# Kernel tuning notes

Measured on AMD Instinct MI355X. Metric: run time of the kernel, lower is better.

## Reference

```python
import jax, jax.numpy as jnp
import numpy as np

N_NODES = 50000
N_EDGES = 800000
IN_DIM = 256
HIDDEN = 32
HEADS = 4
OUT_DIM = 64


def setup_inputs() -> dict:
    key = jax.random.key(0)
    k1, k2, k3, k4, k5, k6, k7 = jax.random.split(key, 7)
    h = jax.random.normal(k1, (N_NODES, IN_DIM), dtype=jnp.float32)
    src = jax.random.randint(k2, (N_EDGES,), 0, N_NODES, dtype=jnp.int32)
    dst = jax.random.randint(k3, (N_EDGES,), 0, N_NODES, dtype=jnp.int32)
    # xavier_normal with relu gain, per-head weights
    gain = float(np.sqrt(2.0))
    W1 = gain * jnp.sqrt(2.0 / (IN_DIM + HIDDEN)) * jax.random.normal(k4, (HEADS, IN_DIM, HIDDEN), dtype=jnp.float32)
    a1 = gain * jnp.sqrt(2.0 / (2 * HIDDEN + 1)) * jax.random.normal(k5, (HEADS, 2 * HIDDEN), dtype=jnp.float32)
    W2 = gain * jnp.sqrt(2.0 / (HIDDEN * HEADS + OUT_DIM)) * jax.random.normal(k6, (1, HIDDEN * HEADS, OUT_DIM), dtype=jnp.float32)
    a2 = gain * jnp.sqrt(2.0 / (2 * OUT_DIM + 1)) * jax.random.normal(k7, (1, 2 * OUT_DIM), dtype=jnp.float32)
    return {"h": h, "src": src, "dst": dst, "W1": W1, "a1": a1, "W2": W2, "a2": a2}


def _gat_layer(x, src, dst, W, a):
    # x: [N, in], W: [H, in, d], a: [H, 2d]
    N = x.shape[0]
    d = W.shape[-1]
    z = jnp.einsum('ni,hio->nho', x, W)                    # [N, H, d]
    a_s, a_d = a[:, :d], a[:, d:]
    es = jnp.einsum('nho,ho->nh', z, a_s)                  # per-node src score
    ed = jnp.einsum('nho,ho->nh', z, a_d)                  # per-node dst score
    e = jax.nn.leaky_relu(es[src] + ed[dst])               # [E, H]
    # segment (per-destination) softmax over incoming edges
    emax = jax.ops.segment_max(e, dst, num_segments=N)     # [N, H]
    ex = jnp.exp(e - emax[dst])
    denom = jax.ops.segment_sum(ex, dst, num_segments=N)   # [N, H]
    alpha = ex / denom[dst]                                # [E, H]
    # scatter weighted sum of source feats back to destinations
    out = jax.ops.segment_sum(alpha[:, :, None] * z[src], dst, num_segments=N)  # [N, H, d]
    return out.reshape(N, -1)


def reference(h, src, dst, W1, a1, W2, a2):
    h1 = jax.nn.elu(_gat_layer(h, src, dst, W1, a1))       # [N, HEADS*HIDDEN]
    return _gat_layer(h1, src, dst, W2, a2)                # [N, OUT_DIM]
```

## Files before the change

kernel.cpp:

```cpp
#include <hip/hip_runtime.h>
#include <hip/hip_bf16.h>
#include <math.h>

#define N_NODES 50000
#define N_EDGES 800000
#define IN_DIM 256
#define HID 32
#define HEADS 4
#define OUT_DIM 64

#define SCAN_CHUNK 1024
#define SCAN_BLOCKS ((N_NODES + SCAN_CHUNK - 1) / SCAN_CHUNK)

typedef __attribute__((ext_vector_type(8))) short bf16x8;
typedef __attribute__((ext_vector_type(4))) float f32x4;

__device__ __forceinline__ float lrelu(float e) { return e > 0.f ? e : 0.01f * e; }
__device__ __forceinline__ float bflo(unsigned u) { return __uint_as_float(u << 16); }
__device__ __forceinline__ float bfhi(unsigned u) { return __uint_as_float(u & 0xffff0000u); }

__device__ __forceinline__ unsigned short rne_bf16(float x) {
    unsigned u = __float_as_uint(x);
    unsigned r = u + 0x7fffu + ((u >> 16) & 1u);
    return (unsigned short)(r >> 16);
}

__device__ __forceinline__ void splitf(float x, short& hi, short& lo) {
    unsigned u = __float_as_uint(x);
    unsigned short h = (unsigned short)(u >> 16);
    float hf = __uint_as_float(((unsigned)h) << 16);
    float l = x - hf;
    unsigned short lb = (unsigned short)(__float_as_uint(l) >> 16);
    hi = (short)h;
    lo = (short)lb;
}


__global__ void __launch_bounds__(256) prep_kernel(
        const float* __restrict__ W1, const float* __restrict__ a1,
        const float* __restrict__ W2, const float* __restrict__ a2,
        unsigned short* __restrict__ B1h, unsigned short* __restrict__ B1l,
        unsigned short* __restrict__ B2h, unsigned short* __restrict__ B2l,
        int* __restrict__ count) {
    int gid = blockIdx.x * 256 + threadIdx.x;
    if (gid < N_NODES) count[gid] = 0;

    int k = blockIdx.x;
    int c = threadIdx.x;
    if (c < 144) {
        float val = 0.f;
        if (c < 128) {
            val = W1[(size_t)(c >> 5) * IN_DIM * HID + (size_t)k * HID + (c & 31)];
        } else if (c < 136) {
            int j = c - 128;
            int hd = (j < 4) ? j : (j - 4);
            int off = (j < 4) ? 0 : HID;
            const float* Wp = W1 + (size_t)hd * IN_DIM * HID + (size_t)k * HID;
            const float* ap = a1 + hd * 2 * HID + off;
            float s = 0.f;
            for (int o = 0; o < HID; o++) s += Wp[o] * ap[o];
            val = s;
        }
        unsigned short hi = rne_bf16(val);
        float hf = __uint_as_float(((unsigned)hi) << 16);
        unsigned short lo = rne_bf16(val - hf);
        int s_ = k >> 5, q = (k >> 3) & 3, j8 = k & 7;
        int nt = c >> 4, L = q * 16 + (c & 15);
        size_t idx = (((size_t)s_ * 9 + nt) * 64 + L) * 8 + j8;
        B1h[idx] = hi;
        B1l[idx] = lo;
    } else if (c >= 160 && c < 240 && k < 128) {
        int c2 = c - 160;
        float val = 0.f;
        if (c2 < 64) {
            val = W2[(size_t)k * OUT_DIM + c2];
        } else if (c2 < 66) {
            const float* ap = a2 + (c2 - 64) * OUT_DIM;
            const float* Wp = W2 + (size_t)k * OUT_DIM;
            float s = 0.f;
            for (int o = 0; o < OUT_DIM; o++) s += Wp[o] * ap[o];
            val = s;
        }
        unsigned short hi = rne_bf16(val);
        float hf = __uint_as_float(((unsigned)hi) << 16);
        unsigned short lo = rne_bf16(val - hf);
        int s_ = k >> 5, q = (k >> 3) & 3, j8 = k & 7;
        int nt = c2 >> 4, L = q * 16 + (c2 & 15);
        size_t idx = (((size_t)s_ * 5 + nt) * 64 + L) * 8 + j8;
        B2h[idx] = hi;
        B2l[idx] = lo;
    }
}


__global__ void hist_kernel(const int* __restrict__ dst, int* __restrict__ count,
                            int* __restrict__ rank) {
    int i = blockIdx.x * blockDim.x + threadIdx.x;
    if (i < N_EDGES) rank[i] = atomicAdd(&count[dst[i]], 1);
}

__global__ void scan1_kernel(const int* __restrict__ count, int* __restrict__ row_start,
                             int* __restrict__ blocksum) {
    __shared__ int sdata[256];
    int t = threadIdx.x;
    int base = blockIdx.x * SCAN_CHUNK + t * 4;
    int v[4];
    int s = 0;
#pragma unroll
    for (int j = 0; j < 4; j++) {
        int idx = base + j;
        int x = (idx < N_NODES) ? count[idx] : 0;
        v[j] = x;
        s += x;
    }
    sdata[t] = s;
    __syncthreads();
    for (int off = 1; off < 256; off <<= 1) {
        int u = (t >= off) ? sdata[t - off] : 0;
        __syncthreads();
        sdata[t] += u;
        __syncthreads();
    }
    int excl = sdata[t] - s;
#pragma unroll
    for (int j = 0; j < 4; j++) {
        int idx = base + j;
        if (idx < N_NODES) row_start[idx] = excl;
        excl += v[j];
    }
    if (t == 255) blocksum[blockIdx.x] = sdata[255];
}

__global__ void scan23_kernel(int* __restrict__ row_start, const int* __restrict__ blocksum) {
    __shared__ int pre;
    int t = threadIdx.x;
    if (t < 64) {
        int v = (t < SCAN_BLOCKS) ? blocksum[t] : 0;
#pragma unroll
        for (int off = 1; off < 64; off <<= 1) {
            int u = __shfl_up(v, off);
            if (t >= off) v += u;
        }
        if (t == blockIdx.x) pre = v - blocksum[t];
    }
    __syncthreads();
    int add = pre;
    int base = blockIdx.x * SCAN_CHUNK + t * 4;
#pragma unroll
    for (int j = 0; j < 4; j++) {
        int idx = base + j;
        if (idx < N_NODES) row_start[idx] += add;
    }
}

__global__ void scatter_kernel(const int* __restrict__ src, const int* __restrict__ dst,
                               const int* __restrict__ rank, const int* __restrict__ row_start,
                               int* __restrict__ esrc) {
    int i = blockIdx.x * blockDim.x + threadIdx.x;
    if (i < N_EDGES) esrc[row_start[dst[i]] + rank[i]] = src[i];
}


__global__ void __launch_bounds__(256) proj1_mfma(
        const float* __restrict__ h, const unsigned short* __restrict__ Bh,
        const unsigned short* __restrict__ Bl, __hip_bfloat16* __restrict__ z1b,
        float* __restrict__ es1, float* __restrict__ ed1) {
    int tid = threadIdx.x;
    int wave = tid >> 6;
    int L = tid & 63;
    int q = L >> 4, L15 = L & 15;
    int n0 = blockIdx.x * 64 + wave * 16;

    int rowA = n0 + L15;
    int rrA = rowA < N_NODES ? rowA : N_NODES - 1;
    const float* hrow = h + (size_t)rrA * IN_DIM + q * 8;

    f32x4 acc[9];
#pragma unroll
    for (int nt = 0; nt < 9; nt++) acc[nt] = (f32x4)(0.f);

    float4 x0 = *(const float4*)(hrow);
    float4 x1 = *(const float4*)(hrow + 4);

#pragma unroll
    for (int s = 0; s < 8; s++) {
        int sn = (s < 7) ? s + 1 : 7;
        float4 p0 = *(const float4*)(hrow + sn * 32);
        float4 p1 = *(const float4*)(hrow + sn * 32 + 4);

        float xs[8] = {x0.x, x0.y, x0.z, x0.w, x1.x, x1.y, x1.z, x1.w};
        bf16x8 ah, al;
#pragma unroll
        for (int j = 0; j < 8; j++) {
            short hi, lo;
            splitf(xs[j], hi, lo);
            ah[j] = hi;
            al[j] = lo;
        }

        const bf16x8* bhp = (const bf16x8*)(Bh + ((size_t)s * 9 * 64) * 8 + (size_t)L * 8);
        const bf16x8* blp = (const bf16x8*)(Bl + ((size_t)s * 9 * 64) * 8 + (size_t)L * 8);
#pragma unroll
        for (int nt = 0; nt < 9; nt++) {
            bf16x8 bh = bhp[nt * 64];
            acc[nt] = __builtin_amdgcn_mfma_f32_16x16x32_bf16(ah, bh, acc[nt], 0, 0, 0);
            acc[nt] = __builtin_amdgcn_mfma_f32_16x16x32_bf16(al, bh, acc[nt], 0, 0, 0);
        }
        {
            bf16x8 bl8 = blp[8 * 64];
            acc[8] = __builtin_amdgcn_mfma_f32_16x16x32_bf16(ah, bl8, acc[8], 0, 0, 0);
        }
        x0 = p0;
        x1 = p1;
    }

#pragma unroll
    for (int r = 0; r < 4; r++) {
        int rowc = n0 + q * 4 + r;
        if (rowc < N_NODES) {
#pragma unroll
            for (int nt = 0; nt < 8; nt++)
                z1b[(size_t)rowc * 128 + nt * 16 + L15] = __float2bfloat16(acc[nt][r]);
            if (L15 < 4) es1[rowc * HEADS + L15] = acc[8][r];
            else if (L15 < 8) ed1[rowc * HEADS + (L15 - 4)] = acc[8][r];
        }
    }
}


__global__ void __launch_bounds__(256) agg1_kernel(
        const __hip_bfloat16* __restrict__ z1b, const float* __restrict__ es1,
        const float* __restrict__ ed1, const int* __restrict__ row_start,
        const int* __restrict__ count, const int* __restrict__ esrc,
        __hip_bfloat16* __restrict__ h1b) {
    int v = blockIdx.x * 4 + (threadIdx.x >> 6);
    int L = threadIdx.x & 63;
    int sub = L >> 4;
    int c16 = L & 15;
    int hd = c16 >> 2;
    int beg = row_start[v], deg = count[v];
    float edv = ed1[v * HEADS + hd];
    const int* ep = esrc + beg;
    float lacc = 0.f;
    float acc[8];
#pragma unroll
    for (int i = 0; i < 8; i++) acc[i] = 0.f;
    const uint4* zq = (const uint4*)z1b;

    for (int j0 = 0; j0 < deg; j0 += 32) {
        int se[8];
        uint4 u[8];
        float ev[8];
#pragma unroll
        for (int g = 0; g < 8; g++) {
            if (j0 + g * 4 < deg) {
                int e = j0 + g * 4 + sub;
                se[g] = ep[(e < deg) ? e : 0];
            }
        }
#pragma unroll
        for (int g = 0; g < 8; g++) {
            if (j0 + g * 4 < deg) {
                u[g] = zq[(size_t)se[g] * 16 + c16];
                ev[g] = es1[se[g] * HEADS + hd];
            }
        }
#pragma unroll
        for (int g = 0; g < 8; g++) {
            if (j0 + g * 4 < deg) {
                bool val = (j0 + g * 4 + sub) < deg;
                float q = val ? __expf(lrelu(ev[g] + edv)) : 0.f;
                lacc += q;
                acc[0] = fmaf(q, bflo(u[g].x), acc[0]);
                acc[1] = fmaf(q, bfhi(u[g].x), acc[1]);
                acc[2] = fmaf(q, bflo(u[g].y), acc[2]);
                acc[3] = fmaf(q, bfhi(u[g].y), acc[3]);
                acc[4] = fmaf(q, bflo(u[g].z), acc[4]);
                acc[5] = fmaf(q, bfhi(u[g].z), acc[5]);
                acc[6] = fmaf(q, bflo(u[g].w), acc[6]);
                acc[7] = fmaf(q, bfhi(u[g].w), acc[7]);
            }
        }
    }
    lacc += __shfl_xor(lacc, 1);
    lacc += __shfl_xor(lacc, 2);
    lacc += __shfl_xor(lacc, 16);
    lacc += __shfl_xor(lacc, 32);
    lacc *= 0.25f;
#pragma unroll
    for (int i = 0; i < 8; i++) {
        acc[i] += __shfl_xor(acc[i], 16);
        acc[i] += __shfl_xor(acc[i], 32);
    }
    if (L < 16) {
        float inv = (deg > 0) ? 1.f / lacc : 0.f;
        unsigned w[4];
#pragma unroll
        for (int i = 0; i < 4; i++) {
            float r0 = acc[2 * i] * inv;
            float r1 = acc[2 * i + 1] * inv;
            r0 = r0 > 0.f ? r0 : __expf(r0) - 1.f;
            r1 = r1 > 0.f ? r1 : __expf(r1) - 1.f;
            w[i] = (unsigned)rne_bf16(r0) | ((unsigned)rne_bf16(r1) << 16);
        }
        uint4* dst = (uint4*)(h1b + (size_t)v * 128 + c16 * 8);
        *dst = make_uint4(w[0], w[1], w[2], w[3]);
    }
}


__global__ void __launch_bounds__(256) proj2_mfma(
        const __hip_bfloat16* __restrict__ h1b, const unsigned short* __restrict__ Bh,
        const unsigned short* __restrict__ Bl, __hip_bfloat16* __restrict__ z2b,
        float* __restrict__ es2, float* __restrict__ ed2) {
    int tid = threadIdx.x;
    int wave = tid >> 6;
    int L = tid & 63;
    int q = L >> 4, L15 = L & 15;
    int n0 = blockIdx.x * 64 + wave * 16;

    int rowA = n0 + L15;
    int rrA = rowA < N_NODES ? rowA : N_NODES - 1;
    const bf16x8* hq = (const bf16x8*)(h1b + (size_t)rrA * 128);

    f32x4 acc[5];
#pragma unroll
    for (int nt = 0; nt < 5; nt++) acc[nt] = (f32x4)(0.f);

#pragma unroll
    for (int s = 0; s < 4; s++) {
        bf16x8 a = hq[s * 4 + q];
        const bf16x8* bhp = (const bf16x8*)(Bh + ((size_t)s * 5 * 64) * 8 + (size_t)L * 8);
        const bf16x8* blp = (const bf16x8*)(Bl + ((size_t)s * 5 * 64) * 8 + (size_t)L * 8);
#pragma unroll
        for (int nt = 0; nt < 5; nt++)
            acc[nt] = __builtin_amdgcn_mfma_f32_16x16x32_bf16(a, bhp[nt * 64], acc[nt], 0, 0, 0);
        acc[4] = __builtin_amdgcn_mfma_f32_16x16x32_bf16(a, blp[4 * 64], acc[4], 0, 0, 0);
    }

#pragma unroll
    for (int r = 0; r < 4; r++) {
        int rowc = n0 + q * 4 + r;
        if (rowc < N_NODES) {
#pragma unroll
            for (int nt = 0; nt < 4; nt++)
                z2b[(size_t)rowc * OUT_DIM + nt * 16 + L15] = __float2bfloat16(acc[nt][r]);
            if (L15 == 0) es2[rowc] = acc[4][r];
            else if (L15 == 1) ed2[rowc] = acc[4][r];
        }
    }
}


__global__ void __launch_bounds__(256) agg2_kernel(
        const __hip_bfloat16* __restrict__ z2b, const float* __restrict__ es2,
        const float* __restrict__ ed2, const int* __restrict__ row_start,
        const int* __restrict__ count, const int* __restrict__ esrc,
        float* __restrict__ out) {
    int v = blockIdx.x * 4 + (threadIdx.x >> 6);
    int L = threadIdx.x & 63;
    int sub = L >> 3;
    int c8 = L & 7;
    int beg = row_start[v], deg = count[v];
    float edv = ed2[v];
    const int* ep = esrc + beg;
    float lacc = 0.f;
    float acc[8];
#pragma unroll
    for (int i = 0; i < 8; i++) acc[i] = 0.f;
    const uint4* zq = (const uint4*)z2b;

    for (int j0 = 0; j0 < deg; j0 += 32) {
        int se[4];
        uint4 u[4];
        float ev[4];
#pragma unroll
        for (int g = 0; g < 4; g++) {
            if (j0 + g * 8 < deg) {
                int e = j0 + g * 8 + sub;
                se[g] = ep[(e < deg) ? e : 0];
            }
        }
#pragma unroll
        for (int g = 0; g < 4; g++) {
            if (j0 + g * 8 < deg) {
                u[g] = zq[(size_t)se[g] * 8 + c8];
                ev[g] = es2[se[g]];
            }
        }
#pragma unroll
        for (int g = 0; g < 4; g++) {
            if (j0 + g * 8 < deg) {
                bool val = (j0 + g * 8 + sub) < deg;
                float q = val ? __expf(lrelu(ev[g] + edv)) : 0.f;
                lacc += q;
                acc[0] = fmaf(q, bflo(u[g].x), acc[0]);
                acc[1] = fmaf(q, bfhi(u[g].x), acc[1]);
                acc[2] = fmaf(q, bflo(u[g].y), acc[2]);
                acc[3] = fmaf(q, bfhi(u[g].y), acc[3]);
                acc[4] = fmaf(q, bflo(u[g].z), acc[4]);
                acc[5] = fmaf(q, bfhi(u[g].z), acc[5]);
                acc[6] = fmaf(q, bflo(u[g].w), acc[6]);
                acc[7] = fmaf(q, bfhi(u[g].w), acc[7]);
            }
        }
    }
    lacc += __shfl_xor(lacc, 8);
    lacc += __shfl_xor(lacc, 16);
    lacc += __shfl_xor(lacc, 32);
#pragma unroll
    for (int i = 0; i < 8; i++) {
        acc[i] += __shfl_xor(acc[i], 8);
        acc[i] += __shfl_xor(acc[i], 16);
        acc[i] += __shfl_xor(acc[i], 32);
    }
    if (L < 8) {
        float inv = (deg > 0) ? 1.f / lacc : 0.f;
        float4 r0, r1;
#pragma unroll
        for (int i = 0; i < 8; i++) {
            float r = acc[i] * inv;
            if (i < 4) (&r0.x)[i] = r;
            else (&r1.x)[i - 4] = r;
        }
        float* dst = out + (size_t)v * OUT_DIM + c8 * 8;
        *(float4*)dst = r0;
        *(float4*)(dst + 4) = r1;
    }
}


extern "C" void kernel_launch(void* const* d_in, const int* in_sizes, int n_in,
                              void* d_out, int out_size, void* d_ws, size_t ws_size,
                              hipStream_t stream) {
    const float* h  = (const float*)d_in[0];
    const int* src  = (const int*)d_in[1];
    const int* dst  = (const int*)d_in[2];
    const float* W1 = (const float*)d_in[3];
    const float* a1 = (const float*)d_in[4];
    const float* W2 = (const float*)d_in[5];
    const float* a2 = (const float*)d_in[6];
    float* out = (float*)d_out;

    char* w = (char*)d_ws;
    size_t off = 0;
    auto alloc = [&](size_t bytes) {
        void* p = w + off;
        off = (off + bytes + 255) & ~(size_t)255;
        return p;
    };
    __hip_bfloat16* z1b = (__hip_bfloat16*)alloc((size_t)N_NODES * 128 * 2);
    float* es1 = (float*)alloc((size_t)N_NODES * HEADS * 4);
    float* ed1 = (float*)alloc((size_t)N_NODES * HEADS * 4);
    __hip_bfloat16* h1b = (__hip_bfloat16*)alloc((size_t)N_NODES * 128 * 2);
    __hip_bfloat16* z2b = (__hip_bfloat16*)alloc((size_t)N_NODES * OUT_DIM * 2);
    float* es2 = (float*)alloc((size_t)N_NODES * 4);
    float* ed2 = (float*)alloc((size_t)N_NODES * 4);
    int* count     = (int*)alloc((size_t)N_NODES * 4);
    int* row_start = (int*)alloc((size_t)N_NODES * 4);
    int* rank      = (int*)alloc((size_t)N_EDGES * 4);
    int* blocksum  = (int*)alloc((size_t)SCAN_BLOCKS * 4);
    int* esrc      = (int*)alloc((size_t)N_EDGES * 4);
    unsigned short* Bf1h = (unsigned short*)alloc((size_t)8 * 9 * 64 * 8 * 2);
    unsigned short* Bf1l = (unsigned short*)alloc((size_t)8 * 9 * 64 * 8 * 2);
    unsigned short* Bf2h = (unsigned short*)alloc((size_t)4 * 5 * 64 * 8 * 2);
    unsigned short* Bf2l = (unsigned short*)alloc((size_t)4 * 5 * 64 * 8 * 2);

    prep_kernel<<<256, 256, 0, stream>>>(W1, a1, W2, a2, Bf1h, Bf1l, Bf2h, Bf2l, count);
    hist_kernel<<<(N_EDGES + 255) / 256, 256, 0, stream>>>(dst, count, rank);
    scan1_kernel<<<SCAN_BLOCKS, 256, 0, stream>>>(count, row_start, blocksum);
    scan23_kernel<<<SCAN_BLOCKS, 256, 0, stream>>>(row_start, blocksum);
    scatter_kernel<<<(N_EDGES + 255) / 256, 256, 0, stream>>>(src, dst, rank, row_start, esrc);

    const int MBLK = (N_NODES + 63) / 64;
    proj1_mfma<<<MBLK, 256, 0, stream>>>(h, Bf1h, Bf1l, z1b, es1, ed1);
    agg1_kernel<<<N_NODES / 4, 256, 0, stream>>>(z1b, es1, ed1, row_start, count, esrc, h1b);
    proj2_mfma<<<MBLK, 256, 0, stream>>>(h1b, Bf2h, Bf2l, z2b, es2, ed2);
    agg2_kernel<<<N_NODES / 4, 256, 0, stream>>>(z2b, es2, ed2, row_start, count, esrc, out);
}
```

Before: 230.0 us.

## Split GAT aggregation across feature slices with more blocks per node

```diff
diff --git a/kernel.cpp b/kernel.cpp
--- a/kernel.cpp
+++ b/kernel.cpp
@@ -233,13 +233,14 @@
         const float* __restrict__ ed1, const int* __restrict__ row_start,
         const int* __restrict__ count, const int* __restrict__ esrc,
         __hip_bfloat16* __restrict__ h1b) {
-    int v = blockIdx.x * 4 + (threadIdx.x >> 6);
+    int bi = blockIdx.x;
+    int g = bi & 3;
+    int v = (bi >> 2) * 4 + (threadIdx.x >> 6);
     int L = threadIdx.x & 63;
-    int sub = L >> 4;
-    int c16 = L & 15;
-    int hd = c16 >> 2;
+    int e16 = L >> 2;
+    int c4 = L & 3;
     int beg = row_start[v], deg = count[v];
-    float edv = ed1[v * HEADS + hd];
+    float edv = ed1[v * HEADS + g];
     const int* ep = esrc + beg;
     float lacc = 0.f;
     float acc[8];
@@ -248,51 +249,52 @@
     const uint4* zq = (const uint4*)z1b;
 
     for (int j0 = 0; j0 < deg; j0 += 32) {
-        int se[8];
-        uint4 u[8];
-        float ev[8];
-#pragma unroll
-        for (int g = 0; g < 8; g++) {
-            if (j0 + g * 4 < deg) {
-                int e = j0 + g * 4 + sub;
-                se[g] = ep[(e < deg) ? e : 0];
-            }
-        }
-#pragma unroll
-        for (int g = 0; g < 8; g++) {
-            if (j0 + g * 4 < deg) {
-                u[g] = zq[(size_t)se[g] * 16 + c16];
-                ev[g] = es1[se[g] * HEADS + hd];
-            }
-        }
-#pragma unroll
-        for (int g = 0; g < 8; g++) {
-            if (j0 + g * 4 < deg) {
-                bool val = (j0 + g * 4 + sub) < deg;
-                float q = val ? __expf(lrelu(ev[g] + edv)) : 0.f;
+        int se[2];
+        float ev[2];
+        uint4 u[2];
+#pragma unroll
+        for (int t = 0; t < 2; t++) {
+            if (j0 + t * 16 < deg) {
+                int e = j0 + t * 16 + e16;
+                se[t] = ep[(e < deg) ? e : 0];
+            }
+        }
+#pragma unroll
+        for (int t = 0; t < 2; t++) {
+            if (j0 + t * 16 < deg) {
+                u[t] = zq[(size_t)se[t] * 16 + g * 4 + c4];
+                ev[t] = es1[se[t] * HEADS + g];
+            }
+        }
+#pragma unroll
+        for (int t = 0; t < 2; t++) {
+            if (j0 + t * 16 < deg) {
+                bool val = (j0 + t * 16 + e16) < deg;
+                float q = val ? __expf(lrelu(ev[t] + edv)) : 0.f;
                 lacc += q;
-                acc[0] = fmaf(q, bflo(u[g].x), acc[0]);
-                acc[1] = fmaf(q, bfhi(u[g].x), acc[1]);
-                acc[2] = fmaf(q, bflo(u[g].y), acc[2]);
-                acc[3] = fmaf(q, bfhi(u[g].y), acc[3]);
-                acc[4] = fmaf(q, bflo(u[g].z), acc[4]);
-                acc[5] = fmaf(q, bfhi(u[g].z), acc[5]);
-                acc[6] = fmaf(q, bflo(u[g].w), acc[6]);
-                acc[7] = fmaf(q, bfhi(u[g].w), acc[7]);
-            }
-        }
-    }
-    lacc += __shfl_xor(lacc, 1);
-    lacc += __shfl_xor(lacc, 2);
+                acc[0] = fmaf(q, bflo(u[t].x), acc[0]);
+                acc[1] = fmaf(q, bfhi(u[t].x), acc[1]);
+                acc[2] = fmaf(q, bflo(u[t].y), acc[2]);
+                acc[3] = fmaf(q, bfhi(u[t].y), acc[3]);
+                acc[4] = fmaf(q, bflo(u[t].z), acc[4]);
+                acc[5] = fmaf(q, bfhi(u[t].z), acc[5]);
+                acc[6] = fmaf(q, bflo(u[t].w), acc[6]);
+                acc[7] = fmaf(q, bfhi(u[t].w), acc[7]);
+            }
+        }
+    }
+    lacc += __shfl_xor(lacc, 4);
+    lacc += __shfl_xor(lacc, 8);
     lacc += __shfl_xor(lacc, 16);
     lacc += __shfl_xor(lacc, 32);
-    lacc *= 0.25f;
 #pragma unroll
     for (int i = 0; i < 8; i++) {
+        acc[i] += __shfl_xor(acc[i], 4);
+        acc[i] += __shfl_xor(acc[i], 8);
         acc[i] += __shfl_xor(acc[i], 16);
         acc[i] += __shfl_xor(acc[i], 32);
     }
-    if (L < 16) {
+    if (L < 4) {
         float inv = (deg > 0) ? 1.f / lacc : 0.f;
         unsigned w[4];
 #pragma unroll
@@ -303,7 +305,7 @@
             r1 = r1 > 0.f ? r1 : __expf(r1) - 1.f;
             w[i] = (unsigned)rne_bf16(r0) | ((unsigned)rne_bf16(r1) << 16);
         }
-        uint4* dst = (uint4*)(h1b + (size_t)v * 128 + c16 * 8);
+        uint4* dst = (uint4*)(h1b + (size_t)v * 128 + g * 32 + L * 8);
         *dst = make_uint4(w[0], w[1], w[2], w[3]);
     }
 }
@@ -357,10 +359,12 @@
         const float* __restrict__ ed2, const int* __restrict__ row_start,
         const int* __restrict__ count, const int* __restrict__ esrc,
         float* __restrict__ out) {
-    int v = blockIdx.x * 4 + (threadIdx.x >> 6);
+    int bi = blockIdx.x;
+    int g = bi & 1;
+    int v = (bi >> 1) * 4 + (threadIdx.x >> 6);
     int L = threadIdx.x & 63;
-    int sub = L >> 3;
-    int c8 = L & 7;
+    int e16 = L >> 2;
+    int c4 = L & 3;
     int beg = row_start[v], deg = count[v];
     float edv = ed2[v];
     const int* ep = esrc + beg;
@@ -371,50 +375,52 @@
     const uint4* zq = (const uint4*)z2b;
 
     for (int j0 = 0; j0 < deg; j0 += 32) {
-        int se[4];
-        uint4 u[4];
-        float ev[4];
-#pragma unroll
-        for (int g = 0; g < 4; g++) {
-            if (j0 + g * 8 < deg) {
-                int e = j0 + g * 8 + sub;
-                se[g] = ep[(e < deg) ? e : 0];
-            }
-        }
-#pragma unroll
-        for (int g = 0; g < 4; g++) {
-            if (j0 + g * 8 < deg) {
-                u[g] = zq[(size_t)se[g] * 8 + c8];
-                ev[g] = es2[se[g]];
-            }
-        }
-#pragma unroll
-        for (int g = 0; g < 4; g++) {
-            if (j0 + g * 8 < deg) {
-                bool val = (j0 + g * 8 + sub) < deg;
-                float q = val ? __expf(lrelu(ev[g] + edv)) : 0.f;
+        int se[2];
+        float ev[2];
+        uint4 u[2];
+#pragma unroll
+        for (int t = 0; t < 2; t++) {
+            if (j0 + t * 16 < deg) {
+                int e = j0 + t * 16 + e16;
+                se[t] = ep[(e < deg) ? e : 0];
+            }
+        }
+#pragma unroll
+        for (int t = 0; t < 2; t++) {
+            if (j0 + t * 16 < deg) {
+                u[t] = zq[(size_t)se[t] * 8 + g * 4 + c4];
+                ev[t] = es2[se[t]];
+            }
+        }
+#pragma unroll
+        for (int t = 0; t < 2; t++) {
+            if (j0 + t * 16 < deg) {
+                bool val = (j0 + t * 16 + e16) < deg;
+                float q = val ? __expf(lrelu(ev[t] + edv)) : 0.f;
                 lacc += q;
-                acc[0] = fmaf(q, bflo(u[g].x), acc[0]);
-                acc[1] = fmaf(q, bfhi(u[g].x), acc[1]);
-                acc[2] = fmaf(q, bflo(u[g].y), acc[2]);
-                acc[3] = fmaf(q, bfhi(u[g].y), acc[3]);
-                acc[4] = fmaf(q, bflo(u[g].z), acc[4]);
-                acc[5] = fmaf(q, bfhi(u[g].z), acc[5]);
-                acc[6] = fmaf(q, bflo(u[g].w), acc[6]);
-                acc[7] = fmaf(q, bfhi(u[g].w), acc[7]);
-            }
-        }
-    }
+                acc[0] = fmaf(q, bflo(u[t].x), acc[0]);
+                acc[1] = fmaf(q, bfhi(u[t].x), acc[1]);
+                acc[2] = fmaf(q, bflo(u[t].y), acc[2]);
+                acc[3] = fmaf(q, bfhi(u[t].y), acc[3]);
+                acc[4] = fmaf(q, bflo(u[t].z), acc[4]);
+                acc[5] = fmaf(q, bfhi(u[t].z), acc[5]);
+                acc[6] = fmaf(q, bflo(u[t].w), acc[6]);
+                acc[7] = fmaf(q, bfhi(u[t].w), acc[7]);
+            }
+        }
+    }
+    lacc += __shfl_xor(lacc, 4);
     lacc += __shfl_xor(lacc, 8);
     lacc += __shfl_xor(lacc, 16);
     lacc += __shfl_xor(lacc, 32);
 #pragma unroll
     for (int i = 0; i < 8; i++) {
+        acc[i] += __shfl_xor(acc[i], 4);
         acc[i] += __shfl_xor(acc[i], 8);
         acc[i] += __shfl_xor(acc[i], 16);
         acc[i] += __shfl_xor(acc[i], 32);
     }
-    if (L < 8) {
+    if (L < 4) {
         float inv = (deg > 0) ? 1.f / lacc : 0.f;
         float4 r0, r1;
 #pragma unroll
@@ -423,7 +429,7 @@
             if (i < 4) (&r0.x)[i] = r;
             else (&r1.x)[i - 4] = r;
         }
-        float* dst = out + (size_t)v * OUT_DIM + c8 * 8;
+        float* dst = out + (size_t)v * OUT_DIM + g * 32 + L * 8;
         *(float4*)dst = r0;
         *(float4*)(dst + 4) = r1;
     }
@@ -474,7 +480,7 @@
 
     const int MBLK = (N_NODES + 63) / 64;
     proj1_mfma<<<MBLK, 256, 0, stream>>>(h, Bf1h, Bf1l, z1b, es1, ed1);
-    agg1_kernel<<<N_NODES / 4, 256, 0, stream>>>(z1b, es1, ed1, row_start, count, esrc, h1b);
+    agg1_kernel<<<(N_NODES / 4) * 4, 256, 0, stream>>>(z1b, es1, ed1, row_start, count, esrc, h1b);
     proj2_mfma<<<MBLK, 256, 0, stream>>>(h1b, Bf2h, Bf2l, z2b, es2, ed2);
-    agg2_kernel<<<N_NODES / 4, 256, 0, stream>>>(z2b, es2, ed2, row_start, count, esrc, out);
-}
+    agg2_kernel<<<(N_NODES / 4) * 2, 256, 0, stream>>>(z2b, es2, ed2, row_start, count, esrc, out);
+}
```

After: 300.8 us. 30.8% more time.
